# Kernel tuning notes

Hardware: AMD Instinct MI355X
Metric: run time of the kernel (lower is better)

Reference implementation:

```python
import jax, jax.numpy as jnp
import numpy as np

THRESHOLD = 0.1
N_HEAD = 16
NEG_INF = -1e9


def setup_inputs() -> dict:
    key = jax.random.key(0)
    ks = jax.random.split(key, 8)
    B, T, C = 2, 2048, 1024
    H, D, R = N_HEAD, C // N_HEAD, 8
    return {
        "x": jax.random.normal(ks[0], (B, T, C), dtype=jnp.float32),
        "W_attn": jax.random.normal(ks[1], (C, 3 * C), dtype=jnp.float32) * 0.02,
        "W_proj": jax.random.normal(ks[2], (C, C), dtype=jnp.float32) * 0.02,
        "W_recip": jax.random.normal(ks[3], (D, R), dtype=jnp.float32) * 0.02,
        "w_std": jax.random.uniform(ks[4], (H,), dtype=jnp.float32),
        "w_rec": jax.random.uniform(ks[5], (H,), dtype=jnp.float32),
        "w_disc": jax.random.uniform(ks[6], (H,), dtype=jnp.float32),
        "d_bias": jax.random.normal(ks[7], (H, T), dtype=jnp.float32) * 0.02,
    }


def reference(x, W_attn, W_proj, W_recip, w_std, w_rec, w_disc, d_bias):
    B, T, C = x.shape
    H = N_HEAD
    D = C // H
    R = W_recip.shape[1]
    D_std = D - R

    # QKV projection (Linear without bias)
    qkv = x @ W_attn  # [B,T,3C]
    q, k, v = jnp.split(qkv, 3, axis=2)

    def to_heads(t):
        return t.reshape(B, T, H, D).transpose(0, 2, 1, 3)  # [B,H,T,D]

    q, k, v = to_heads(q), to_heads(k), to_heads(v)

    # low-rank reciprocal projections
    QW = q @ W_recip  # [B,H,T,R]
    KW = k @ W_recip

    ws = jnp.sqrt(jnp.clip(w_std, 1e-8))[:, None, None]  # [H,1,1]
    wr = jnp.sqrt(jnp.clip(w_rec, 1e-8))[:, None, None]
    use_ra = (w_rec > THRESHOLD)[:, None, None]  # [H,1,1]

    # RA heads: augmented Q/K = [ws*Q_std | wr*KW] / [ws*K_std | wr*QW]
    q_aug = jnp.concatenate([ws * q[..., :D_std], wr * KW], axis=-1)
    k_aug = jnp.concatenate([ws * k[..., :D_std], wr * QW], axis=-1)
    q_eff = jnp.where(use_ra, q_aug, ws * q)
    k_eff = jnp.where(use_ra, k_aug, ws * k)

    # mean-centered discoverability column bias: [1,H,1,T]
    d = d_bias[:, :T]
    d = d - d.mean(axis=-1, keepdims=True)
    bias = (d * w_disc[:, None])[None, :, None, :]

    scale = 1.0 / jnp.sqrt(jnp.asarray(D, dtype=x.dtype))
    scores = jnp.einsum("bhid,bhjd->bhij", q_eff, k_eff) * scale + bias
    causal = jnp.tril(jnp.ones((T, T), dtype=bool))
    scores = jnp.where(causal[None, None], scores, NEG_INF)
    attn = jax.nn.softmax(scores, axis=-1)
    out = jnp.einsum("bhij,bhjd->bhid", attn, v)  # [B,H,T,D]

    out = out.transpose(0, 2, 1, 3).reshape(B, T, C)
    return out @ W_proj
```

## Files before the change

### kernel.cpp

```cpp
#include <hip/hip_runtime.h>
#include <hip/hip_bf16.h>

#define DEVI __device__ __forceinline__

typedef __attribute__((ext_vector_type(8))) short short8;
typedef __attribute__((ext_vector_type(4))) short short4v;
typedef __attribute__((ext_vector_type(4))) float floatx4;

static constexpr int B_ = 2, T_ = 2048, C_ = 1024, H_ = 16, D_ = 64;
static constexpr float LOG2E = 1.44269504088896f;

DEVI float bf2f(unsigned short u) {
    union { unsigned int i; float f; } v; v.i = ((unsigned int)u) << 16; return v.f;
}
DEVI unsigned short f2bf(float f) {
    union { float f; unsigned int i; } v; v.f = f;
    unsigned int x = v.i;
    return (unsigned short)((x + 0x7fffu + ((x >> 16) & 1u)) >> 16);
}
DEVI unsigned int pk2bf(float lo, float hi) {
#if __has_builtin(__builtin_amdgcn_cvt_pk_bf16_f32)
    typedef __attribute__((ext_vector_type(2))) __bf16 bf16x2;
    union { bf16x2 v; unsigned int u; } r;
    r.v = __builtin_amdgcn_cvt_pk_bf16_f32(lo, hi);
    return r.u;
#else
    return (unsigned int)f2bf(lo) | ((unsigned int)f2bf(hi) << 16);
#endif
}
DEVI float fast_exp2(float x) {
#if __has_builtin(__builtin_amdgcn_exp2f)
    return __builtin_amdgcn_exp2f(x);
#else
    return __expf(x * 0.6931471805599453f);
#endif
}

DEVI void async16(const unsigned short* g, unsigned short* l) {
    __builtin_amdgcn_global_load_lds((const __attribute__((address_space(1))) void*)g,
                                     (__attribute__((address_space(3))) void*)l, 16, 0, 0);
}

DEVI void tr_body(const float* in, unsigned short* out, int K, int N, int bx, int by,
                  int tid, float (*tile)[65]) {
    int k0 = by * 64, n0 = bx * 64;
#pragma unroll
    for (int r = 0; r < 4; r++) {
        int ci = tid + r * 256;
        int row = ci >> 4, c4 = (ci & 15) * 4;
        float4 v = *(const float4*)&in[(size_t)(k0 + row) * N + n0 + c4];
        tile[row][c4 + 0] = v.x; tile[row][c4 + 1] = v.y;
        tile[row][c4 + 2] = v.z; tile[row][c4 + 3] = v.w;
    }
    __syncthreads();
#pragma unroll
    for (int r = 0; r < 2; r++) {
        int ci = tid + r * 256;
        int row = ci >> 3, c8 = (ci & 7) * 8;
        union { unsigned short u[8]; short8 s; } o;
#pragma unroll
        for (int j = 0; j < 8; j++) o.u[j] = f2bf(tile[c8 + j][row]);
        *(short8*)&out[(size_t)(n0 + row) * K + k0 + c8] = o.s;
    }
}

__global__ __launch_bounds__(256) void k_prep(const float* __restrict__ x,
                                              const float* __restrict__ W_attn,
                                              const float* __restrict__ W_proj,
                                              const float* __restrict__ d_bias,
                                              const float* __restrict__ w_disc,
                                              unsigned short* __restrict__ x_bf,
                                              unsigned short* __restrict__ wa_t,
                                              unsigned short* __restrict__ wp_t,
                                              float* __restrict__ bias) {
    __shared__ float tile[64][65];
    __shared__ float red[256];
    int bid = blockIdx.x, tid = threadIdx.x;
    if (bid < 2048) {
        int i = bid * 256 + tid;
        const float4* p = (const float4*)x + (size_t)i * 2;
        float4 a = p[0], b = p[1];
        union { unsigned short u[8]; short8 s; } r;
        r.u[0] = f2bf(a.x); r.u[1] = f2bf(a.y); r.u[2] = f2bf(a.z); r.u[3] = f2bf(a.w);
        r.u[4] = f2bf(b.x); r.u[5] = f2bf(b.y); r.u[6] = f2bf(b.z); r.u[7] = f2bf(b.w);
        *(short8*)&x_bf[(size_t)i * 8] = r.s;
    } else if (bid < 2816) {
        int idx = bid - 2048;
        tr_body(W_attn, wa_t, 1024, 3072, idx % 48, idx / 48, tid, tile);
    } else if (bid < 3072) {
        int idx = bid - 2816;
        tr_body(W_proj, wp_t, 1024, 1024, idx & 15, idx >> 4, tid, tile);
    } else {
        int h = bid - 3072;
        float s = 0.f;
        for (int t = tid; t < T_; t += 256) s += d_bias[h * T_ + t];
        red[tid] = s;
        __syncthreads();
        for (int st = 128; st > 0; st >>= 1) {
            if (tid < st) red[tid] += red[tid + st];
            __syncthreads();
        }
        float mean = red[0] * (1.0f / T_);
        float wd = w_disc[h] * LOG2E;
        for (int t = tid; t < T_; t += 256) bias[h * T_ + t] = (d_bias[h * T_ + t] - mean) * wd;
    }
}

template <typename OUT>
__global__ __launch_bounds__(256) void k_gemm(const unsigned short* __restrict__ A,
                                              const unsigned short* __restrict__ Bt,
                                              OUT* __restrict__ C, int M, int N, int K) {
    __shared__ __align__(16) unsigned short As[128 * 32];
    __shared__ __align__(16) unsigned short Bs[128 * 32];
    int m0 = blockIdx.y * 128, n0 = blockIdx.x * 128;
    int tid = threadIdx.x, l = tid & 63, w = tid >> 6;
    int wm = (w >> 1) * 64, wn = (w & 1) * 64;
    int lm = l & 15, lq = l >> 4;
    floatx4 acc[4][4];
#pragma unroll
    for (int a = 0; a < 4; a++)
#pragma unroll
        for (int b = 0; b < 4; b++) acc[a][b] = {0.f, 0.f, 0.f, 0.f};

    for (int k0 = 0; k0 < K; k0 += 32) {
        __syncthreads();
#pragma unroll
        for (int r = 0; r < 2; r++) {
            int ci = tid + r * 256;
            int row = ci >> 2, off = (ci & 3) * 8;
            async16(&A[(size_t)(m0 + row) * K + k0 + off], &As[row * 32 + off]);
            async16(&Bt[(size_t)(n0 + row) * K + k0 + off], &Bs[row * 32 + off]);
        }
        __syncthreads();
        short8 af[4], bf[4];
#pragma unroll
        for (int t = 0; t < 4; t++) af[t] = *(short8*)&As[(wm + t * 16 + lm) * 32 + lq * 8];
#pragma unroll
        for (int t = 0; t < 4; t++) bf[t] = *(short8*)&Bs[(wn + t * 16 + lm) * 32 + lq * 8];
#pragma unroll
        for (int tm = 0; tm < 4; tm++)
#pragma unroll
            for (int tn = 0; tn < 4; tn++)
                acc[tm][tn] = __builtin_amdgcn_mfma_f32_16x16x32_bf16(af[tm], bf[tn], acc[tm][tn], 0, 0, 0);
    }
#pragma unroll
    for (int tm = 0; tm < 4; tm++)
#pragma unroll
        for (int tn = 0; tn < 4; tn++) {
            int row = m0 + wm + tm * 16 + lq * 4;
            int col = n0 + wn + tn * 16 + lm;
#pragma unroll
            for (int r = 0; r < 4; r++) {
                float v = acc[tm][tn][r];
                if constexpr (sizeof(OUT) == 2) C[(size_t)(row + r) * N + col] = (OUT)f2bf(v);
                else                            C[(size_t)(row + r) * N + col] = v;
            }
        }
}

__global__ __launch_bounds__(256) void k_gemm64(const unsigned short* __restrict__ A,
                                                const unsigned short* __restrict__ Bt,
                                                float* __restrict__ C, int M, int N, int K) {
    __shared__ __align__(16) unsigned short As[128 * 32];
    __shared__ __align__(16) unsigned short Bs[64 * 32];
    int m0 = blockIdx.y * 128, n0 = blockIdx.x * 64;
    int tid = threadIdx.x, l = tid & 63, w = tid >> 6;
    int wm = w * 32;
    int lm = l & 15, lq = l >> 4;
    floatx4 acc[2][4];
#pragma unroll
    for (int a = 0; a < 2; a++)
#pragma unroll
        for (int b = 0; b < 4; b++) acc[a][b] = {0.f, 0.f, 0.f, 0.f};

    for (int k0 = 0; k0 < K; k0 += 32) {
        __syncthreads();
#pragma unroll
        for (int r = 0; r < 2; r++) {
            int ci = tid + r * 256;
            int row = ci >> 2, off = (ci & 3) * 8;
            async16(&A[(size_t)(m0 + row) * K + k0 + off], &As[row * 32 + off]);
        }
        {
            int row = tid >> 2, off = (tid & 3) * 8;
            async16(&Bt[(size_t)(n0 + row) * K + k0 + off], &Bs[row * 32 + off]);
        }
        __syncthreads();
        short8 af[2], bf[4];
#pragma unroll
        for (int t = 0; t < 2; t++) af[t] = *(short8*)&As[(wm + t * 16 + lm) * 32 + lq * 8];
#pragma unroll
        for (int t = 0; t < 4; t++) bf[t] = *(short8*)&Bs[(t * 16 + lm) * 32 + lq * 8];
#pragma unroll
        for (int tm = 0; tm < 2; tm++)
#pragma unroll
            for (int tn = 0; tn < 4; tn++)
                acc[tm][tn] = __builtin_amdgcn_mfma_f32_16x16x32_bf16(af[tm], bf[tn], acc[tm][tn], 0, 0, 0);
    }
#pragma unroll
    for (int tm = 0; tm < 2; tm++)
#pragma unroll
        for (int tn = 0; tn < 4; tn++) {
            int row = m0 + wm + tm * 16 + lq * 4;
            int col = n0 + tn * 16 + lm;
#pragma unroll
            for (int r = 0; r < 4; r++) C[(size_t)(row + r) * N + col] = acc[tm][tn][r];
        }
}

DEVI void build_body(const unsigned short* qkv, const float* Wr, const float* w_std,
                     const float* w_rec, unsigned short* qe, unsigned short* ke, int g) {
    int t = g & (T_ - 1), h = (g >> 11) & (H_ - 1), b = g >> 15;
    float ws = sqrtf(fmaxf(w_std[h], 1e-8f));
    float wr = sqrtf(fmaxf(w_rec[h], 1e-8f));
    bool ra = w_rec[h] > 0.1f;
    const unsigned short* qrow = qkv + (size_t)(b * T_ + t) * 3072 + h * 64;
    const unsigned short* krow = qrow + 1024;
    float q[64], k[64];
#pragma unroll
    for (int i = 0; i < 8; i++) {
        short8 qv = *(const short8*)&qrow[i * 8];
        short8 kv = *(const short8*)&krow[i * 8];
#pragma unroll
        for (int j = 0; j < 8; j++) {
            q[i * 8 + j] = bf2f((unsigned short)qv[j]);
            k[i * 8 + j] = bf2f((unsigned short)kv[j]);
        }
    }
    float QW[8], KW[8];
#pragma unroll
    for (int r = 0; r < 8; r++) { QW[r] = 0.f; KW[r] = 0.f; }
#pragma unroll
    for (int d = 0; d < 64; d++)
#pragma unroll
        for (int r = 0; r < 8; r++) {
            QW[r] += q[d] * Wr[d * 8 + r];
            KW[r] += k[d] * Wr[d * 8 + r];
        }
    const float qscale = 0.125f * LOG2E;
    size_t tbase = (size_t)(b * H_ + h) * 131072 + (size_t)(t >> 4) * 1024 + (size_t)(t & 15) * 8;
#pragma unroll
    for (int i = 0; i < 8; i++) {
        union { unsigned short u[8]; short8 s; } uq, uk;
#pragma unroll
        for (int j = 0; j < 8; j++) {
            int d = i * 8 + j;
            float qv, kv;
            if (ra && d >= 56) { qv = wr * KW[d - 56]; kv = wr * QW[d - 56]; }
            else               { qv = ws * q[d];       kv = ws * k[d]; }
            uq.u[j] = f2bf(qv * qscale);
            uk.u[j] = f2bf(kv);
        }
        size_t off = tbase + (size_t)(i >> 2) * 512 + (size_t)(i & 3) * 128;
        *(short8*)&qe[off] = uq.s;
        *(short8*)&ke[off] = uk.s;
    }
}

__global__ __launch_bounds__(256) void k_bv(const unsigned short* __restrict__ qkv,
                                            const float* __restrict__ W_recip,
                                            const float* __restrict__ w_std,
                                            const float* __restrict__ w_rec,
                                            unsigned short* __restrict__ qe,
                                            unsigned short* __restrict__ ke,
                                            unsigned short* __restrict__ vt) {
    __shared__ float Wr[64 * 8];
    int bid = blockIdx.x, tid = threadIdx.x;
    if (bid < 256) {
        for (int i = tid; i < 512; i += 256) Wr[i] = W_recip[i];
        __syncthreads();
        build_body(qkv, Wr, w_std, w_rec, qe, ke, bid * 256 + tid);
    } else {
        int g = bid - 256;
        int tchunk = g & 63;
        int h = (g >> 6) & 15, b = g >> 10;
        int d = tid & 63, tg = tid >> 6;
        int t0 = tchunk * 32 + tg * 8;
        union { unsigned short u[8]; short8 s; } v;
#pragma unroll
        for (int i = 0; i < 8; i++)
            v.u[i] = qkv[(size_t)(b * T_ + t0 + i) * 3072 + 2048 + h * 64 + d];
        size_t off = (size_t)((b * H_ + h)) * 131072 + (size_t)tchunk * 2048 +
                     (size_t)(d >> 4) * 512 + (size_t)tg * 128 + (size_t)(d & 15) * 8;
        *(short8*)&vt[off] = v.s;
    }
}

DEVI void online_softmax(float sv[4][4], float& m_i, float& l_i, floatx4* O,
                         unsigned int pk[4][2]) {
    float mx = sv[0][0];
#pragma unroll
    for (int js = 0; js < 4; js++)
#pragma unroll
        for (int r = 0; r < 4; r++) mx = fmaxf(mx, sv[js][r]);
    mx = fmaxf(mx, __shfl_xor(mx, 16));
    mx = fmaxf(mx, __shfl_xor(mx, 32));
    float mn = fmaxf(m_i, mx);
    float alpha = fast_exp2(m_i - mn);
    m_i = mn;
    float rs = 0.f;
#pragma unroll
    for (int js = 0; js < 4; js++)
#pragma unroll
        for (int r = 0; r < 4; r++) {
            float p = fast_exp2(sv[js][r] - mn);
            sv[js][r] = p;
            rs += p;
        }
    rs += __shfl_xor(rs, 16);
    rs += __shfl_xor(rs, 32);
    l_i = l_i * alpha + rs;
#pragma unroll
    for (int dt = 0; dt < 4; dt++) {
        floatx4 o = O[dt];
        o[0] *= alpha; o[1] *= alpha; o[2] *= alpha; o[3] *= alpha;
        O[dt] = o;
    }
#pragma unroll
    for (int js = 0; js < 4; js++) {
        pk[js][0] = pk2bf(sv[js][0], sv[js][1]);
        pk[js][1] = pk2bf(sv[js][2], sv[js][3]);
    }
}

DEVI short8 make_pf(const unsigned int pk[4][2], int c, int srcLo, int srcHi, bool hi) {
    int a0 = __shfl((int)pk[2 * c][0], srcLo);
    int a1 = __shfl((int)pk[2 * c][1], srcLo);
    int a2 = __shfl((int)pk[2 * c][0], srcHi);
    int a3 = __shfl((int)pk[2 * c][1], srcHi);
    int b0 = __shfl((int)pk[2 * c + 1][0], srcLo);
    int b1 = __shfl((int)pk[2 * c + 1][1], srcLo);
    int b2 = __shfl((int)pk[2 * c + 1][0], srcHi);
    int b3 = __shfl((int)pk[2 * c + 1][1], srcHi);
    union { int i[4]; short8 s; } pf;
    pf.i[0] = hi ? b0 : a0;
    pf.i[1] = hi ? b1 : a1;
    pf.i[2] = hi ? b2 : a2;
    pf.i[3] = hi ? b3 : a3;
    return pf.s;
}

struct KF { short8 lo[4]; short8 hi[4]; };

__global__ __launch_bounds__(256, 2) void k_attn(const unsigned short* __restrict__ qe,
                                                 const unsigned short* __restrict__ ke,
                                                 const unsigned short* __restrict__ vt,
                                                 const float* __restrict__ bias,
                                                 unsigned short* __restrict__ obf) {
    int bh = blockIdx.y;
    int b = bh >> 4, h = bh & 15;
    int tid = threadIdx.x, l = tid & 63, w = tid >> 6;
    int lm = l & 15, lq = l >> 4;
    int l8 = l * 8;
    const size_t hb = (size_t)bh * 131072;
    const unsigned short* qeh = qe + hb;
    const unsigned short* keh = ke + hb;
    const unsigned short* vth = vt + hb;
    const float* biash = bias + h * T_;

    int gA = blockIdx.x * 4 + w;
    int gB = 127 - gA;
    int itA = (gA >> 2) + 1, itB = (gB >> 2) + 1;
    int irowA = gA * 16 + lm, irowB = gB * 16 + lm;

    short8 qA0 = *(const short8*)(qeh + (size_t)gA * 1024 + l8);
    short8 qA1 = *(const short8*)(qeh + (size_t)gA * 1024 + 512 + l8);
    short8 qB0 = *(const short8*)(qeh + (size_t)gB * 1024 + l8);
    short8 qB1 = *(const short8*)(qeh + (size_t)gB * 1024 + 512 + l8);

    floatx4 OA[4], OB[4];
#pragma unroll
    for (int i = 0; i < 4; i++) { OA[i] = {0.f, 0.f, 0.f, 0.f}; OB[i] = {0.f, 0.f, 0.f, 0.f}; }
    float mA = -3e38f, lA = 0.f, mB = -3e38f, lB = 0.f;

    const int srcLo = ((lq & 1) * 2) * 16 + lm;
    const int srcHi = srcLo + 16;
    const bool hi = (lq >> 1) & 1;

    KF kfa, kfb;
#pragma unroll
    for (int js = 0; js < 4; js++) {
        const unsigned short* kp = keh + (size_t)js * 1024 + l8;
        kfa.lo[js] = *(const short8*)kp;
        kfa.hi[js] = *(const short8*)(kp + 512);
    }

    auto step = [&](int s, KF& cur, KF& nxt) {
        int j0 = s * 64;
        bool doA = (s < itA);
        bool maskA = (s == itA - 1);
        bool maskB = (s == itB - 1);
        {
            const unsigned short* kb = keh + (size_t)(s + 1) * 4096 + l8;
#pragma unroll
            for (int js = 0; js < 4; js++) {
                nxt.lo[js] = *(const short8*)(kb + js * 1024);
                nxt.hi[js] = *(const short8*)(kb + js * 1024 + 512);
            }
        }
        short8 vfr[2][4];
#pragma unroll
        for (int c = 0; c < 2; c++)
#pragma unroll
            for (int dt = 0; dt < 4; dt++)
                vfr[c][dt] = *(const short8*)(vth + (size_t)((j0 >> 5) + c) * 2048 + dt * 512 + l8);
        floatx4 sb4[4], sa4[4];
#pragma unroll
        for (int js = 0; js < 4; js++) {
            floatx4 sb = {0.f, 0.f, 0.f, 0.f};
            sb = __builtin_amdgcn_mfma_f32_16x16x32_bf16(cur.lo[js], qB0, sb, 0, 0, 0);
            sb = __builtin_amdgcn_mfma_f32_16x16x32_bf16(cur.hi[js], qB1, sb, 0, 0, 0);
            sb4[js] = sb;
        }
        if (doA) {
#pragma unroll
            for (int js = 0; js < 4; js++) {
                floatx4 sa = {0.f, 0.f, 0.f, 0.f};
                sa = __builtin_amdgcn_mfma_f32_16x16x32_bf16(cur.lo[js], qA0, sa, 0, 0, 0);
                sa = __builtin_amdgcn_mfma_f32_16x16x32_bf16(cur.hi[js], qA1, sa, 0, 0, 0);
                sa4[js] = sa;
            }
        }
        float bv[4][4];
#pragma unroll
        for (int js = 0; js < 4; js++) {
            float4 bj = *(const float4*)&biash[j0 + js * 16 + lq * 4];
            bv[js][0] = bj.x; bv[js][1] = bj.y; bv[js][2] = bj.z; bv[js][3] = bj.w;
        }
        float svB[4][4];
#pragma unroll
        for (int js = 0; js < 4; js++)
#pragma unroll
            for (int r = 0; r < 4; r++) svB[js][r] = sb4[js][r] + bv[js][r];
        if (maskB) {
#pragma unroll
            for (int js = 0; js < 4; js++) {
                int jb = j0 + js * 16 + lq * 4;
#pragma unroll
                for (int r = 0; r < 4; r++)
                    if (jb + r > irowB) svB[js][r] = -1e9f;
            }
        }
        unsigned int pkB[4][2];
        online_softmax(svB, mB, lB, OB, pkB);

        if (doA) {
            float svA[4][4];
#pragma unroll
            for (int js = 0; js < 4; js++)
#pragma unroll
                for (int r = 0; r < 4; r++) svA[js][r] = sa4[js][r] + bv[js][r];
            if (maskA) {
#pragma unroll
                for (int js = 0; js < 4; js++) {
                    int jb = j0 + js * 16 + lq * 4;
#pragma unroll
                    for (int r = 0; r < 4; r++)
                        if (jb + r > irowA) svA[js][r] = -1e9f;
                }
            }
            unsigned int pkA[4][2];
            online_softmax(svA, mA, lA, OA, pkA);
#pragma unroll
            for (int c = 0; c < 2; c++) {
                short8 pfA = make_pf(pkA, c, srcLo, srcHi, hi);
                short8 pfB = make_pf(pkB, c, srcLo, srcHi, hi);
#pragma unroll
                for (int dt = 0; dt < 4; dt++) {
                    OA[dt] = __builtin_amdgcn_mfma_f32_16x16x32_bf16(vfr[c][dt], pfA, OA[dt], 0, 0, 0);
                    OB[dt] = __builtin_amdgcn_mfma_f32_16x16x32_bf16(vfr[c][dt], pfB, OB[dt], 0, 0, 0);
                }
            }
        } else {
#pragma unroll
            for (int c = 0; c < 2; c++) {
                short8 pfB = make_pf(pkB, c, srcLo, srcHi, hi);
#pragma unroll
                for (int dt = 0; dt < 4; dt++)
                    OB[dt] = __builtin_amdgcn_mfma_f32_16x16x32_bf16(vfr[c][dt], pfB, OB[dt], 0, 0, 0);
            }
        }
    };

    int s = 0;
    for (; s + 2 <= itB; s += 2) {
        step(s, kfa, kfb);
        step(s + 1, kfb, kfa);
    }
    if (s < itB) step(s, kfa, kfb);

    {
        float inv = 1.0f / lA;
        unsigned short* orow = obf + (size_t)(b * T_ + irowA) * C_ + h * 64;
#pragma unroll
        for (int dt = 0; dt < 4; dt++) {
            union { unsigned short u[4]; short4v s4; } o;
#pragma unroll
            for (int r = 0; r < 4; r++) o.u[r] = f2bf(OA[dt][r] * inv);
            *(short4v*)&orow[dt * 16 + lq * 4] = o.s4;
        }
    }
    {
        float inv = 1.0f / lB;
        unsigned short* orow = obf + (size_t)(b * T_ + irowB) * C_ + h * 64;
#pragma unroll
        for (int dt = 0; dt < 4; dt++) {
            union { unsigned short u[4]; short4v s4; } o;
#pragma unroll
            for (int r = 0; r < 4; r++) o.u[r] = f2bf(OB[dt][r] * inv);
            *(short4v*)&orow[dt * 16 + lq * 4] = o.s4;
        }
    }
}

extern "C" void kernel_launch(void* const* d_in, const int* in_sizes, int n_in,
                              void* d_out, int out_size, void* d_ws, size_t ws_size,
                              hipStream_t stream) {
    const float* x       = (const float*)d_in[0];
    const float* W_attn  = (const float*)d_in[1];
    const float* W_proj  = (const float*)d_in[2];
    const float* W_recip = (const float*)d_in[3];
    const float* w_std   = (const float*)d_in[4];
    const float* w_rec   = (const float*)d_in[5];
    const float* w_disc  = (const float*)d_in[6];
    const float* d_bias  = (const float*)d_in[7];

    char* ws = (char*)d_ws;
    size_t o = 0;
    unsigned short* x_bf = (unsigned short*)(ws + o); o += (size_t)4096 * 1024 * 2;
    unsigned short* wa_t = (unsigned short*)(ws + o); o += (size_t)3072 * 1024 * 2;
    unsigned short* wp_t = (unsigned short*)(ws + o); o += (size_t)1024 * 1024 * 2;
    unsigned short* qkv  = (unsigned short*)(ws + o); o += (size_t)4096 * 3072 * 2;
    unsigned short* qe   = (unsigned short*)(ws + o); o += (size_t)32 * 2048 * 64 * 2;
    unsigned short* ke   = (unsigned short*)(ws + o); o += (size_t)32 * 2048 * 64 * 2;
    unsigned short* vt   = (unsigned short*)(ws + o); o += (size_t)32 * 2048 * 64 * 2;
    unsigned short* obf  = (unsigned short*)(ws + o); o += (size_t)4096 * 1024 * 2;
    float* bias          = (float*)(ws + o);          o += (size_t)16 * 2048 * 4;

    k_prep<<<3088, 256, 0, stream>>>(x, W_attn, W_proj, d_bias, w_disc, x_bf, wa_t, wp_t, bias);
    k_gemm<unsigned short><<<dim3(24, 32), 256, 0, stream>>>(x_bf, wa_t, qkv, 4096, 3072, 1024);
    k_bv<<<2304, 256, 0, stream>>>(qkv, W_recip, w_std, w_rec, qe, ke, vt);
    k_attn<<<dim3(16, 32), 256, 0, stream>>>(qe, ke, vt, bias, obf);
    k_gemm64<<<dim3(16, 32), 256, 0, stream>>>(obf, wp_t, (float*)d_out, 4096, 1024, 1024);
}
```

Measured before the change: 209.7 us.

## Split attention KV range across warp pairs and split-K the output projection

The attention kernel now assigns two query-tile pairs per block and has two warps per pair process alternating KV blocks. Their partial softmax state is merged through shared memory, which doubles the grid and raises the occupancy target. The output projection becomes a 128x128-tile split-K GEMM with two K slices accumulated by atomic adds into a zeroed output, adding a memset launch. This aims to raise parallelism and occupancy, at the cost of atomic traffic, an extra memset, and register pressure under launch_bounds(256,4).

```diff
diff --git a/kernel.cpp b/kernel.cpp
--- a/kernel.cpp
+++ b/kernel.cpp
@@ -158,53 +158,53 @@
         }
 }
 
-__global__ __launch_bounds__(256) void k_gemm64(const unsigned short* __restrict__ A,
-                                                const unsigned short* __restrict__ Bt,
-                                                float* __restrict__ C, int M, int N, int K) {
+__global__ __launch_bounds__(256) void k_gemm_sk(const unsigned short* __restrict__ A,
+                                                 const unsigned short* __restrict__ Bt,
+                                                 float* __restrict__ C, int M, int N, int K,
+                                                 int KS) {
     __shared__ __align__(16) unsigned short As[128 * 32];
-    __shared__ __align__(16) unsigned short Bs[64 * 32];
-    int m0 = blockIdx.y * 128, n0 = blockIdx.x * 64;
+    __shared__ __align__(16) unsigned short Bs[128 * 32];
+    int m0 = blockIdx.y * 128, n0 = blockIdx.x * 128;
+    int ks0 = blockIdx.z * KS;
     int tid = threadIdx.x, l = tid & 63, w = tid >> 6;
-    int wm = w * 32;
+    int wm = (w >> 1) * 64, wn = (w & 1) * 64;
     int lm = l & 15, lq = l >> 4;
-    floatx4 acc[2][4];
-#pragma unroll
-    for (int a = 0; a < 2; a++)
+    floatx4 acc[4][4];
+#pragma unroll
+    for (int a = 0; a < 4; a++)
 #pragma unroll
         for (int b = 0; b < 4; b++) acc[a][b] = {0.f, 0.f, 0.f, 0.f};
 
-    for (int k0 = 0; k0 < K; k0 += 32) {
+    for (int k0 = ks0; k0 < ks0 + KS; k0 += 32) {
         __syncthreads();
 #pragma unroll
         for (int r = 0; r < 2; r++) {
             int ci = tid + r * 256;
             int row = ci >> 2, off = (ci & 3) * 8;
             async16(&A[(size_t)(m0 + row) * K + k0 + off], &As[row * 32 + off]);
-        }
-        {
-            int row = tid >> 2, off = (tid & 3) * 8;
             async16(&Bt[(size_t)(n0 + row) * K + k0 + off], &Bs[row * 32 + off]);
         }
         __syncthreads();
-        short8 af[2], bf[4];
-#pragma unroll
-        for (int t = 0; t < 2; t++) af[t] = *(short8*)&As[(wm + t * 16 + lm) * 32 + lq * 8];
-#pragma unroll
-        for (int t = 0; t < 4; t++) bf[t] = *(short8*)&Bs[(t * 16 + lm) * 32 + lq * 8];
-#pragma unroll
-        for (int tm = 0; tm < 2; tm++)
+        short8 af[4], bf[4];
+#pragma unroll
+        for (int t = 0; t < 4; t++) af[t] = *(short8*)&As[(wm + t * 16 + lm) * 32 + lq * 8];
+#pragma unroll
+        for (int t = 0; t < 4; t++) bf[t] = *(short8*)&Bs[(wn + t * 16 + lm) * 32 + lq * 8];
+#pragma unroll
+        for (int tm = 0; tm < 4; tm++)
 #pragma unroll
             for (int tn = 0; tn < 4; tn++)
                 acc[tm][tn] = __builtin_amdgcn_mfma_f32_16x16x32_bf16(af[tm], bf[tn], acc[tm][tn], 0, 0, 0);
     }
 #pragma unroll
-    for (int tm = 0; tm < 2; tm++)
+    for (int tm = 0; tm < 4; tm++)
 #pragma unroll
         for (int tn = 0; tn < 4; tn++) {
             int row = m0 + wm + tm * 16 + lq * 4;
-            int col = n0 + tn * 16 + lm;
-#pragma unroll
-            for (int r = 0; r < 4; r++) C[(size_t)(row + r) * N + col] = acc[tm][tn][r];
+            int col = n0 + wn + tn * 16 + lm;
+#pragma unroll
+            for (int r = 0; r < 4; r++)
+                unsafeAtomicAdd(&C[(size_t)(row + r) * N + col], acc[tm][tn][r]);
         }
 }
 
@@ -342,14 +342,16 @@
 
 struct KF { short8 lo[4]; short8 hi[4]; };
 
-__global__ __launch_bounds__(256, 2) void k_attn(const unsigned short* __restrict__ qe,
+__global__ __launch_bounds__(256, 4) void k_attn(const unsigned short* __restrict__ qe,
                                                  const unsigned short* __restrict__ ke,
                                                  const unsigned short* __restrict__ vt,
                                                  const float* __restrict__ bias,
                                                  unsigned short* __restrict__ obf) {
+    __shared__ float mrg[2][64][37];
     int bh = blockIdx.y;
     int b = bh >> 4, h = bh & 15;
     int tid = threadIdx.x, l = tid & 63, w = tid >> 6;
+    int p = w & 1, hf = w >> 1;
     int lm = l & 15, lq = l >> 4;
     int l8 = l * 8;
     const size_t hb = (size_t)bh * 131072;
@@ -358,7 +360,7 @@
     const unsigned short* vth = vt + hb;
     const float* biash = bias + h * T_;
 
-    int gA = blockIdx.x * 4 + w;
+    int gA = blockIdx.x * 2 + p;
     int gB = 127 - gA;
     int itA = (gA >> 2) + 1, itB = (gB >> 2) + 1;
     int irowA = gA * 16 + lm, irowB = gB * 16 + lm;
@@ -378,11 +380,13 @@
     const bool hi = (lq >> 1) & 1;
 
     KF kfa, kfb;
-#pragma unroll
-    for (int js = 0; js < 4; js++) {
-        const unsigned short* kp = keh + (size_t)js * 1024 + l8;
-        kfa.lo[js] = *(const short8*)kp;
-        kfa.hi[js] = *(const short8*)(kp + 512);
+    {
+        const unsigned short* kb = keh + (size_t)hf * 4096 + l8;
+#pragma unroll
+        for (int js = 0; js < 4; js++) {
+            kfa.lo[js] = *(const short8*)(kb + js * 1024);
+            kfa.hi[js] = *(const short8*)(kb + js * 1024 + 512);
+        }
     }
 
     auto step = [&](int s, KF& cur, KF& nxt) {
@@ -391,7 +395,7 @@
         bool maskA = (s == itA - 1);
         bool maskB = (s == itB - 1);
         {
-            const unsigned short* kb = keh + (size_t)(s + 1) * 4096 + l8;
+            const unsigned short* kb = keh + (size_t)(s + 2) * 4096 + l8;
 #pragma unroll
             for (int js = 0; js < 4; js++) {
                 nxt.lo[js] = *(const short8*)(kb + js * 1024);
@@ -482,33 +486,62 @@
         }
     };
 
-    int s = 0;
-    for (; s + 2 <= itB; s += 2) {
+    int s = hf;
+    for (; s + 4 <= itB; s += 4) {
         step(s, kfa, kfb);
-        step(s + 1, kfb, kfa);
-    }
-    if (s < itB) step(s, kfa, kfb);
-
-    {
-        float inv = 1.0f / lA;
-        unsigned short* orow = obf + (size_t)(b * T_ + irowA) * C_ + h * 64;
-#pragma unroll
-        for (int dt = 0; dt < 4; dt++) {
-            union { unsigned short u[4]; short4v s4; } o;
-#pragma unroll
-            for (int r = 0; r < 4; r++) o.u[r] = f2bf(OA[dt][r] * inv);
-            *(short4v*)&orow[dt * 16 + lq * 4] = o.s4;
-        }
-    }
-    {
-        float inv = 1.0f / lB;
-        unsigned short* orow = obf + (size_t)(b * T_ + irowB) * C_ + h * 64;
-#pragma unroll
-        for (int dt = 0; dt < 4; dt++) {
-            union { unsigned short u[4]; short4v s4; } o;
-#pragma unroll
-            for (int r = 0; r < 4; r++) o.u[r] = f2bf(OB[dt][r] * inv);
-            *(short4v*)&orow[dt * 16 + lq * 4] = o.s4;
+        step(s + 2, kfb, kfa);
+    }
+    if (s < itB) {
+        step(s, kfa, kfb);
+        s += 2;
+        if (s < itB) step(s, kfb, kfa);
+    }
+
+    if (hf == 1) {
+        float* dst = mrg[p][l];
+#pragma unroll
+        for (int dt = 0; dt < 4; dt++)
+#pragma unroll
+            for (int r = 0; r < 4; r++) {
+                dst[dt * 4 + r] = OA[dt][r];
+                dst[16 + dt * 4 + r] = OB[dt][r];
+            }
+        dst[32] = mA; dst[33] = lA; dst[34] = mB; dst[35] = lB;
+    }
+    __syncthreads();
+    if (hf == 0) {
+        const float* src = mrg[p][l];
+        {
+            float m2 = src[32], l2 = src[33];
+            float m = fmaxf(mA, m2);
+            float f1 = fast_exp2(mA - m), f2 = fast_exp2(m2 - m);
+            float lt = lA * f1 + l2 * f2;
+            float inv = 1.0f / lt;
+            unsigned short* orow = obf + (size_t)(b * T_ + irowA) * C_ + h * 64;
+#pragma unroll
+            for (int dt = 0; dt < 4; dt++) {
+                union { unsigned short u[4]; short4v s4; } o;
+#pragma unroll
+                for (int r = 0; r < 4; r++)
+                    o.u[r] = f2bf((OA[dt][r] * f1 + src[dt * 4 + r] * f2) * inv);
+                *(short4v*)&orow[dt * 16 + lq * 4] = o.s4;
+            }
+        }
+        {
+            float m2 = src[34], l2 = src[35];
+            float m = fmaxf(mB, m2);
+            float f1 = fast_exp2(mB - m), f2 = fast_exp2(m2 - m);
+            float lt = lB * f1 + l2 * f2;
+            float inv = 1.0f / lt;
+            unsigned short* orow = obf + (size_t)(b * T_ + irowB) * C_ + h * 64;
+#pragma unroll
+            for (int dt = 0; dt < 4; dt++) {
+                union { unsigned short u[4]; short4v s4; } o;
+#pragma unroll
+                for (int r = 0; r < 4; r++)
+                    o.u[r] = f2bf((OB[dt][r] * f1 + src[16 + dt * 4 + r] * f2) * inv);
+                *(short4v*)&orow[dt * 16 + lq * 4] = o.s4;
+            }
         }
     }
 }
@@ -540,6 +573,7 @@
     k_prep<<<3088, 256, 0, stream>>>(x, W_attn, W_proj, d_bias, w_disc, x_bf, wa_t, wp_t, bias);
     k_gemm<unsigned short><<<dim3(24, 32), 256, 0, stream>>>(x_bf, wa_t, qkv, 4096, 3072, 1024);
     k_bv<<<2304, 256, 0, stream>>>(qkv, W_recip, w_std, w_rec, qe, ke, vt);
-    k_attn<<<dim3(16, 32), 256, 0, stream>>>(qe, ke, vt, bias, obf);
-    k_gemm64<<<dim3(16, 32), 256, 0, stream>>>(obf, wp_t, (float*)d_out, 4096, 1024, 1024);
-}
+    k_attn<<<dim3(32, 32), 256, 0, stream>>>(qe, ke, vt, bias, obf);
+    hipMemsetAsync(d_out, 0, (size_t)out_size * 4, stream);
+    k_gemm_sk<<<dim3(8, 32, 2), 256, 0, stream>>>(obf, wp_t, (float*)d_out, 4096, 1024, 1024, 512);
+}
```

Measured after the change: 535.0 us. 2.55x slower.

## Simplify attention to one query tile per wave with doubled grid

Applied to the files above, without the earlier changes.

Replaces the paired-tile scheme, where each wave handled a short and a long causal query tile and shared K/V fragment loads between them, with one 16-row query tile per wave and a grid twice as large. It also drops the software double-buffering of K fragments, folds the bias into the MFMA accumulator init, and removes the occupancy hint from launch bounds. The aim is to cut register pressure and raise occupancy and block count for better load spreading across the GPU. In exchange, K/V reuse across two tiles is lost, so K/V traffic roughly doubles, and load balance now relies on the hardware scheduler because per-block work is uneven under causal masking.

```diff
diff --git a/kernel.cpp b/kernel.cpp
--- a/kernel.cpp
+++ b/kernel.cpp
@@ -340,13 +340,11 @@
     return pf.s;
 }
 
-struct KF { short8 lo[4]; short8 hi[4]; };
-
-__global__ __launch_bounds__(256, 2) void k_attn(const unsigned short* __restrict__ qe,
-                                                 const unsigned short* __restrict__ ke,
-                                                 const unsigned short* __restrict__ vt,
-                                                 const float* __restrict__ bias,
-                                                 unsigned short* __restrict__ obf) {
+__global__ __launch_bounds__(256) void k_attn(const unsigned short* __restrict__ qe,
+                                              const unsigned short* __restrict__ ke,
+                                              const unsigned short* __restrict__ vt,
+                                              const float* __restrict__ bias,
+                                              unsigned short* __restrict__ obf) {
     int bh = blockIdx.y;
     int b = bh >> 4, h = bh & 15;
     int tid = threadIdx.x, l = tid & 63, w = tid >> 6;
@@ -358,158 +356,69 @@
     const unsigned short* vth = vt + hb;
     const float* biash = bias + h * T_;
 
-    int gA = blockIdx.x * 4 + w;
-    int gB = 127 - gA;
-    int itA = (gA >> 2) + 1, itB = (gB >> 2) + 1;
-    int irowA = gA * 16 + lm, irowB = gB * 16 + lm;
-
-    short8 qA0 = *(const short8*)(qeh + (size_t)gA * 1024 + l8);
-    short8 qA1 = *(const short8*)(qeh + (size_t)gA * 1024 + 512 + l8);
-    short8 qB0 = *(const short8*)(qeh + (size_t)gB * 1024 + l8);
-    short8 qB1 = *(const short8*)(qeh + (size_t)gB * 1024 + 512 + l8);
-
-    floatx4 OA[4], OB[4];
-#pragma unroll
-    for (int i = 0; i < 4; i++) { OA[i] = {0.f, 0.f, 0.f, 0.f}; OB[i] = {0.f, 0.f, 0.f, 0.f}; }
-    float mA = -3e38f, lA = 0.f, mB = -3e38f, lB = 0.f;
+    int g = 127 - (blockIdx.x * 4 + w);
+    int it = (g >> 2) + 1;
+    int irow = g * 16 + lm;
+
+    short8 q0 = *(const short8*)(qeh + (size_t)g * 1024 + l8);
+    short8 q1 = *(const short8*)(qeh + (size_t)g * 1024 + 512 + l8);
+
+    floatx4 O[4];
+#pragma unroll
+    for (int i = 0; i < 4; i++) O[i] = {0.f, 0.f, 0.f, 0.f};
+    float m_i = -3e38f, l_i = 0.f;
 
     const int srcLo = ((lq & 1) * 2) * 16 + lm;
     const int srcHi = srcLo + 16;
     const bool hi = (lq >> 1) & 1;
 
-    KF kfa, kfb;
-#pragma unroll
-    for (int js = 0; js < 4; js++) {
-        const unsigned short* kp = keh + (size_t)js * 1024 + l8;
-        kfa.lo[js] = *(const short8*)kp;
-        kfa.hi[js] = *(const short8*)(kp + 512);
-    }
-
-    auto step = [&](int s, KF& cur, KF& nxt) {
+    for (int s = 0; s < it; s++) {
         int j0 = s * 64;
-        bool doA = (s < itA);
-        bool maskA = (s == itA - 1);
-        bool maskB = (s == itB - 1);
-        {
-            const unsigned short* kb = keh + (size_t)(s + 1) * 4096 + l8;
-#pragma unroll
-            for (int js = 0; js < 4; js++) {
-                nxt.lo[js] = *(const short8*)(kb + js * 1024);
-                nxt.hi[js] = *(const short8*)(kb + js * 1024 + 512);
-            }
-        }
-        short8 vfr[2][4];
-#pragma unroll
-        for (int c = 0; c < 2; c++)
-#pragma unroll
-            for (int dt = 0; dt < 4; dt++)
-                vfr[c][dt] = *(const short8*)(vth + (size_t)((j0 >> 5) + c) * 2048 + dt * 512 + l8);
-        floatx4 sb4[4], sa4[4];
-#pragma unroll
-        for (int js = 0; js < 4; js++) {
-            floatx4 sb = {0.f, 0.f, 0.f, 0.f};
-            sb = __builtin_amdgcn_mfma_f32_16x16x32_bf16(cur.lo[js], qB0, sb, 0, 0, 0);
-            sb = __builtin_amdgcn_mfma_f32_16x16x32_bf16(cur.hi[js], qB1, sb, 0, 0, 0);
-            sb4[js] = sb;
-        }
-        if (doA) {
-#pragma unroll
-            for (int js = 0; js < 4; js++) {
-                floatx4 sa = {0.f, 0.f, 0.f, 0.f};
-                sa = __builtin_amdgcn_mfma_f32_16x16x32_bf16(cur.lo[js], qA0, sa, 0, 0, 0);
-                sa = __builtin_amdgcn_mfma_f32_16x16x32_bf16(cur.hi[js], qA1, sa, 0, 0, 0);
-                sa4[js] = sa;
-            }
-        }
-        float bv[4][4];
+        const unsigned short* kb = keh + (size_t)s * 4096 + l8;
+        float sv[4][4];
 #pragma unroll
         for (int js = 0; js < 4; js++) {
             float4 bj = *(const float4*)&biash[j0 + js * 16 + lq * 4];
-            bv[js][0] = bj.x; bv[js][1] = bj.y; bv[js][2] = bj.z; bv[js][3] = bj.w;
-        }
-        float svB[4][4];
-#pragma unroll
-        for (int js = 0; js < 4; js++)
-#pragma unroll
-            for (int r = 0; r < 4; r++) svB[js][r] = sb4[js][r] + bv[js][r];
-        if (maskB) {
+            floatx4 sa = {bj.x, bj.y, bj.z, bj.w};
+            short8 kf0 = *(const short8*)(kb + js * 1024);
+            short8 kf1 = *(const short8*)(kb + js * 1024 + 512);
+            sa = __builtin_amdgcn_mfma_f32_16x16x32_bf16(kf0, q0, sa, 0, 0, 0);
+            sa = __builtin_amdgcn_mfma_f32_16x16x32_bf16(kf1, q1, sa, 0, 0, 0);
+            sv[js][0] = sa[0]; sv[js][1] = sa[1]; sv[js][2] = sa[2]; sv[js][3] = sa[3];
+        }
+        short8 vfr[2][4];
+#pragma unroll
+        for (int c = 0; c < 2; c++)
+#pragma unroll
+            for (int dt = 0; dt < 4; dt++)
+                vfr[c][dt] = *(const short8*)(vth + (size_t)(2 * s + c) * 2048 + dt * 512 + l8);
+        if (s == it - 1) {
 #pragma unroll
             for (int js = 0; js < 4; js++) {
                 int jb = j0 + js * 16 + lq * 4;
 #pragma unroll
                 for (int r = 0; r < 4; r++)
-                    if (jb + r > irowB) svB[js][r] = -1e9f;
+                    if (jb + r > irow) sv[js][r] = -1e9f;
             }
         }
-        unsigned int pkB[4][2];
-        online_softmax(svB, mB, lB, OB, pkB);
-
-        if (doA) {
-            float svA[4][4];
-#pragma unroll
-            for (int js = 0; js < 4; js++)
-#pragma unroll
-                for (int r = 0; r < 4; r++) svA[js][r] = sa4[js][r] + bv[js][r];
-            if (maskA) {
-#pragma unroll
-                for (int js = 0; js < 4; js++) {
-                    int jb = j0 + js * 16 + lq * 4;
-#pragma unroll
-                    for (int r = 0; r < 4; r++)
-                        if (jb + r > irowA) svA[js][r] = -1e9f;
-                }
-            }
-            unsigned int pkA[4][2];
-            online_softmax(svA, mA, lA, OA, pkA);
-#pragma unroll
-            for (int c = 0; c < 2; c++) {
-                short8 pfA = make_pf(pkA, c, srcLo, srcHi, hi);
-                short8 pfB = make_pf(pkB, c, srcLo, srcHi, hi);
-#pragma unroll
-                for (int dt = 0; dt < 4; dt++) {
-                    OA[dt] = __builtin_amdgcn_mfma_f32_16x16x32_bf16(vfr[c][dt], pfA, OA[dt], 0, 0, 0);
-                    OB[dt] = __builtin_amdgcn_mfma_f32_16x16x32_bf16(vfr[c][dt], pfB, OB[dt], 0, 0, 0);
-                }
-            }
-        } else {
-#pragma unroll
-            for (int c = 0; c < 2; c++) {
-                short8 pfB = make_pf(pkB, c, srcLo, srcHi, hi);
-#pragma unroll
-                for (int dt = 0; dt < 4; dt++)
-                    OB[dt] = __builtin_amdgcn_mfma_f32_16x16x32_bf16(vfr[c][dt], pfB, OB[dt], 0, 0, 0);
-            }
-        }
-    };
-
-    int s = 0;
-    for (; s + 2 <= itB; s += 2) {
-        step(s, kfa, kfb);
-        step(s + 1, kfb, kfa);
-    }
-    if (s < itB) step(s, kfa, kfb);
-
-    {
-        float inv = 1.0f / lA;
-        unsigned short* orow = obf + (size_t)(b * T_ + irowA) * C_ + h * 64;
-#pragma unroll
-        for (int dt = 0; dt < 4; dt++) {
-            union { unsigned short u[4]; short4v s4; } o;
-#pragma unroll
-            for (int r = 0; r < 4; r++) o.u[r] = f2bf(OA[dt][r] * inv);
-            *(short4v*)&orow[dt * 16 + lq * 4] = o.s4;
-        }
-    }
-    {
-        float inv = 1.0f / lB;
-        unsigned short* orow = obf + (size_t)(b * T_ + irowB) * C_ + h * 64;
-#pragma unroll
-        for (int dt = 0; dt < 4; dt++) {
-            union { unsigned short u[4]; short4v s4; } o;
-#pragma unroll
-            for (int r = 0; r < 4; r++) o.u[r] = f2bf(OB[dt][r] * inv);
-            *(short4v*)&orow[dt * 16 + lq * 4] = o.s4;
-        }
+        unsigned int pk[4][2];
+        online_softmax(sv, m_i, l_i, O, pk);
+#pragma unroll
+        for (int c = 0; c < 2; c++) {
+            short8 pf = make_pf(pk, c, srcLo, srcHi, hi);
+#pragma unroll
+            for (int dt = 0; dt < 4; dt++)
+                O[dt] = __builtin_amdgcn_mfma_f32_16x16x32_bf16(vfr[c][dt], pf, O[dt], 0, 0, 0);
+        }
+    }
+    float inv = 1.0f / l_i;
+    unsigned short* orow = obf + (size_t)(b * T_ + irow) * C_ + h * 64;
+#pragma unroll
+    for (int dt = 0; dt < 4; dt++) {
+        union { unsigned short u[4]; short4v s4; } o;
+#pragma unroll
+        for (int r = 0; r < 4; r++) o.u[r] = f2bf(O[dt][r] * inv);
+        *(short4v*)&orow[dt * 16 + lq * 4] = o.s4;
     }
 }
 
@@ -540,6 +449,6 @@
     k_prep<<<3088, 256, 0, stream>>>(x, W_attn, W_proj, d_bias, w_disc, x_bf, wa_t, wp_t, bias);
     k_gemm<unsigned short><<<dim3(24, 32), 256, 0, stream>>>(x_bf, wa_t, qkv, 4096, 3072, 1024);
     k_bv<<<2304, 256, 0, stream>>>(qkv, W_recip, w_std, w_rec, qe, ke, vt);
-    k_attn<<<dim3(16, 32), 256, 0, stream>>>(qe, ke, vt, bias, obf);
+    k_attn<<<dim3(32, 32), 256, 0, stream>>>(qe, ke, vt, bias, obf);
     k_gemm64<<<dim3(16, 32), 256, 0, stream>>>(obf, wp_t, (float*)d_out, 4096, 1024, 1024);
 }
```

Result: slower. 243.2 us (+15.9%).
